# Kernel tuning notes

Measured on AMD Instinct MI355X. Metric: run time of the kernel, lower is better.

## Reference

```python
import jax, jax.numpy as jnp
import numpy as np

N, S, B, C = 8192, 13, 2, 3
EPS = 1e-6
LAMBDA_COORD, LAMBDA_OBJ, LAMBDA_NOOBJ, LAMBDA_CLASS = 5.0, 1.0, 0.5, 1.0


def setup_inputs() -> dict:
    key = jax.random.key(0)
    k1, k2, k3, k4 = jax.random.split(key, 4)
    predictions = jax.random.normal(k1, (N, S, S, B * (5 + C)), dtype=jnp.float32)
    xywh = jax.random.uniform(k2, (N, S, S, 4), dtype=jnp.float32)
    conf = (jax.random.uniform(k3, (N, S, S)) < 0.3).astype(jnp.float32)  # binary objectness
    cls_idx = jax.random.randint(k4, (N, S, S), 0, C)
    onehot = jax.nn.one_hot(cls_idx, C, dtype=jnp.float32)
    targets = jnp.concatenate(
        [xywh, conf[..., None], jnp.zeros((N, S, S, 5), jnp.float32), onehot], axis=-1
    )  # (N,S,S,13)
    return {"predictions": predictions, "targets": targets}


def reference(predictions, targets):
    batch = predictions.shape[0]
    mask = targets[..., 4] > 0  # (N,S,S) object-present mask
    m = mask.astype(predictions.dtype)

    # --- coord loss (box 0 only, as in the torch loop) ---
    px = jax.nn.sigmoid(predictions[..., 0])
    py = jax.nn.sigmoid(predictions[..., 1])
    pw, ph = predictions[..., 2], predictions[..., 3]
    tx, ty, tw, th = (targets[..., k] for k in range(4))
    coord = (
        (px - tx) ** 2
        + (py - ty) ** 2
        + (jnp.sqrt(jnp.abs(pw) + EPS) - jnp.sqrt(jnp.abs(tw) + EPS)) ** 2
        + (jnp.sqrt(jnp.abs(ph) + EPS) - jnp.sqrt(jnp.abs(th) + EPS)) ** 2
    )
    coord_loss = jnp.sum(m * coord)

    # --- objectness BCE (box 0) on object cells ---
    z = predictions[..., 4]
    tc = targets[..., 4]
    bce_obj = -(tc * jax.nn.log_sigmoid(z) + (1.0 - tc) * jax.nn.log_sigmoid(-z))
    conf_loss_obj = jnp.sum(m * bce_obj)

    # --- no-object BCE on both boxes (target 0) ---
    z_all = predictions[..., jnp.array([4, 9])]  # (N,S,S,B) conf logits
    bce_noobj = -jax.nn.log_sigmoid(-z_all)  # BCE(sigmoid(z), 0)
    conf_loss_noobj = jnp.sum((1.0 - m)[..., None] * bce_noobj)

    # --- class CE on object cells ---
    logits = predictions[..., B * 5 : B * 5 + C]  # (N,S,S,C)
    tcls = jnp.argmax(targets[..., B * 5 : B * 5 + C], axis=-1)
    ce = jax.nn.logsumexp(logits, axis=-1) - jnp.take_along_axis(
        logits, tcls[..., None], axis=-1
    )[..., 0]
    class_loss = jnp.sum(m * ce)

    # normalize by batch only if any such cell exists (matches torch branching)
    n_obj = jnp.sum(mask)
    n_noobj = mask.size - n_obj
    div_obj = jnp.where(n_obj > 0, 1.0 / batch, 1.0)
    div_noobj = jnp.where(n_noobj > 0, 1.0 / batch, 1.0)

    total = (
        LAMBDA_COORD * coord_loss * div_obj
        + LAMBDA_OBJ * conf_loss_obj * div_obj
        + LAMBDA_NOOBJ * conf_loss_noobj * div_noobj
        + LAMBDA_CLASS * class_loss * div_obj
    )
    return total
```

## Files before the change

### kernel.cpp

```cpp
#include <hip/hip_runtime.h>
#include <math.h>


#define EPSV 1e-6f

__global__ __launch_bounds__(256) void phobia_partial(
    const float* __restrict__ pred, const float* __restrict__ tgt,
    float* __restrict__ ws, long long cells)
{
    long long idx0 = (long long)blockIdx.x * blockDim.x + threadIdx.x;
    long long stride = (long long)gridDim.x * blockDim.x;

    float accA = 0.f;
    float accB = 0.f;
    float accC = 0.f;

    for (long long i = idx0; i < cells; i += stride) {
        const float* pr = pred + i * 16;
        const float* tr = tgt  + i * 13;

        float4 p03   = *reinterpret_cast<const float4*>(pr);
        float  p4    = pr[4];
        float  p9    = pr[9];
        float2 p1011 = *reinterpret_cast<const float2*>(pr + 10);
        float  p12   = pr[12];

        float t0 = tr[0], t1 = tr[1], t2 = tr[2], t3 = tr[3], t4 = tr[4];
        float t10 = tr[10], t11 = tr[11], t12 = tr[12];

        float m = (t4 > 0.f) ? 1.f : 0.f;

        float px = 1.f / (1.f + __expf(-p03.x));
        float py = 1.f / (1.f + __expf(-p03.y));
        float dx = px - t0;
        float dy = py - t1;
        float dw = sqrtf(fabsf(p03.z) + EPSV) - sqrtf(fabsf(t2) + EPSV);
        float dh = sqrtf(fabsf(p03.w) + EPSV) - sqrtf(fabsf(t3) + EPSV);
        float coord = dx*dx + dy*dy + dw*dw + dh*dh;

        float l1p4 = __logf(1.f + __expf(-fabsf(p4)));
        float logsig_p4 = fminf(p4, 0.f) - l1p4;
        float logsig_m4 = fminf(-p4, 0.f) - l1p4;
        float bce_obj = -(t4 * logsig_p4 + (1.f - t4) * logsig_m4);
        float bce_no4 = -logsig_m4;
        float bce_no9 = fmaxf(p9, 0.f) + __logf(1.f + __expf(-fabsf(p9)));

        int tcls = 0; float bt = t10;
        if (t11 > bt) { bt = t11; tcls = 1; }
        if (t12 > bt) { tcls = 2; }
        float lt = (tcls == 0) ? p1011.x : ((tcls == 1) ? p1011.y : p12);
        float mx = fmaxf(p1011.x, fmaxf(p1011.y, p12));
        float lse = mx + __logf(__expf(p1011.x - mx) + __expf(p1011.y - mx) + __expf(p12 - mx));
        float ce = lse - lt;

        accA += m * (5.f * coord + bce_obj + ce);
        accB += (1.f - m) * (bce_no4 + bce_no9);
        accC += m;
    }

    #pragma unroll
    for (int o = 32; o > 0; o >>= 1) {
        accA += __shfl_down(accA, o, 64);
        accB += __shfl_down(accB, o, 64);
        accC += __shfl_down(accC, o, 64);
    }
    __shared__ float sA[4], sB[4], sC[4];
    int wave = threadIdx.x >> 6;
    int lane = threadIdx.x & 63;
    if (lane == 0) { sA[wave] = accA; sB[wave] = accB; sC[wave] = accC; }
    __syncthreads();
    if (threadIdx.x == 0) {
        ws[blockIdx.x * 3 + 0] = sA[0] + sA[1] + sA[2] + sA[3];
        ws[blockIdx.x * 3 + 1] = sB[0] + sB[1] + sB[2] + sB[3];
        ws[blockIdx.x * 3 + 2] = sC[0] + sC[1] + sC[2] + sC[3];
    }
}

__global__ __launch_bounds__(1024) void phobia_final(
    const float* __restrict__ ws, int nblocks, float* __restrict__ out, long long cells)
{
    float a = 0.f, b = 0.f, c = 0.f;
    for (int i = threadIdx.x; i < nblocks; i += 1024) {
        a += ws[i * 3 + 0];
        b += ws[i * 3 + 1];
        c += ws[i * 3 + 2];
    }
    #pragma unroll
    for (int o = 32; o > 0; o >>= 1) {
        a += __shfl_down(a, o, 64);
        b += __shfl_down(b, o, 64);
        c += __shfl_down(c, o, 64);
    }
    __shared__ float sA[16], sB[16], sC[16];
    int wave = threadIdx.x >> 6;
    int lane = threadIdx.x & 63;
    if (lane == 0) { sA[wave] = a; sB[wave] = b; sC[wave] = c; }
    __syncthreads();
    if (threadIdx.x == 0) {
        float A = 0.f, B = 0.f, C = 0.f;
        #pragma unroll
        for (int w = 0; w < 16; ++w) { A += sA[w]; B += sB[w]; C += sC[w]; }
        float batch = (float)(cells / 169);
        float invb = 1.f / batch;
        float div_obj   = (C > 0.f) ? invb : 1.f;
        float div_noobj = (C < (float)cells) ? invb : 1.f;
        out[0] = A * div_obj + 0.5f * B * div_noobj;
    }
}

extern "C" void kernel_launch(void* const* d_in, const int* in_sizes, int n_in,
                              void* d_out, int out_size, void* d_ws, size_t ws_size,
                              hipStream_t stream) {
    const float* pred = (const float*)d_in[0];
    const float* tgt  = (const float*)d_in[1];
    float* out = (float*)d_out;
    float* ws  = (float*)d_ws;

    long long cells = (long long)in_sizes[0] / 16;

    int blocks = (int)((cells + 255) / 256);
    size_t need = (size_t)blocks * 3 * sizeof(float);
    while (need > ws_size && blocks > 1) { blocks >>= 1; need = (size_t)blocks * 3 * sizeof(float); }

    phobia_partial<<<blocks, 256, 0, stream>>>(pred, tgt, ws, cells);
    phobia_final<<<1, 1024, 0, stream>>>(ws, blocks, out, cells);
}
```

Baseline: 32.71 us.

## Stage prediction and target chunks through LDS with coalesced float4 loads

Each block now loads a 256-cell chunk of predictions and targets using fully coalesced float4 reads, scatters the needed prediction fields into shared memory, and then has each thread compute its cell from LDS. This replaces the strided per-thread loads, which fetched scattered fields with poor coalescing, especially for the 13-float target rows. In exchange it adds shared-memory traffic, two barriers per chunk, and LDS bank conflicts from the stride-9 and stride-13 layouts. It also assumes the cell count is a multiple of 256 and drops any tail.

```diff
diff --git a/kernel.cpp b/kernel.cpp
--- a/kernel.cpp
+++ b/kernel.cpp
@@ -3,39 +3,54 @@
 
 
 #define EPSV 1e-6f
+#define CHUNK 256
+#define NSLOT 9
 
 __global__ __launch_bounds__(256) void phobia_partial(
     const float* __restrict__ pred, const float* __restrict__ tgt,
-    float* __restrict__ ws, long long cells)
+    float* __restrict__ ws, int nchunks)
 {
-    long long idx0 = (long long)blockIdx.x * blockDim.x + threadIdx.x;
-    long long stride = (long long)gridDim.x * blockDim.x;
+    __shared__ float sp[CHUNK * NSLOT];
+    __shared__ float st[CHUNK * 13];
 
-    float accA = 0.f;
-    float accB = 0.f;
-    float accC = 0.f;
+    const int t = threadIdx.x;
+    float accA = 0.f, accB = 0.f, accC = 0.f;
 
-    for (long long i = idx0; i < cells; i += stride) {
-        const float* pr = pred + i * 16;
-        const float* tr = tgt  + i * 13;
+    for (int chunk = blockIdx.x; chunk < nchunks; chunk += gridDim.x) {
+        const float4* pf4 = reinterpret_cast<const float4*>(pred) + (size_t)chunk * (CHUNK * 4);
+        #pragma unroll
+        for (int s = 0; s < 4; ++s) {
+            int f = s * 256 + t;
+            float4 v = pf4[f];
+            int cell = f >> 2, quad = f & 3;
+            float* dst = &sp[cell * NSLOT];
+            if (quad == 0)      { dst[0] = v.x; dst[1] = v.y; dst[2] = v.z; dst[3] = v.w; }
+            else if (quad == 1) { dst[4] = v.x; }
+            else if (quad == 2) { dst[5] = v.y; dst[6] = v.z; dst[7] = v.w; }
+            else                { dst[8] = v.x; }
+        }
+        const float4* tf4 = reinterpret_cast<const float4*>(tgt) + (size_t)chunk * (CHUNK * 13 / 4);
+        float4* stf4 = reinterpret_cast<float4*>(st);
+        #pragma unroll
+        for (int s = 0; s < 3; ++s) stf4[s * 256 + t] = tf4[s * 256 + t];
+        if (t < 64) stf4[768 + t] = tf4[768 + t];
+        __syncthreads();
 
-        float4 p03   = *reinterpret_cast<const float4*>(pr);
-        float  p4    = pr[4];
-        float  p9    = pr[9];
-        float2 p1011 = *reinterpret_cast<const float2*>(pr + 10);
-        float  p12   = pr[12];
-
+        const float* pp = &sp[t * NSLOT];
+        const float* tr = &st[t * 13];
+        float p0 = pp[0], p1 = pp[1], p2 = pp[2], p3 = pp[3], p4 = pp[4];
+        float p9 = pp[5], p10 = pp[6], p11 = pp[7], p12 = pp[8];
         float t0 = tr[0], t1 = tr[1], t2 = tr[2], t3 = tr[3], t4 = tr[4];
         float t10 = tr[10], t11 = tr[11], t12 = tr[12];
 
         float m = (t4 > 0.f) ? 1.f : 0.f;
 
-        float px = 1.f / (1.f + __expf(-p03.x));
-        float py = 1.f / (1.f + __expf(-p03.y));
+        float px = 1.f / (1.f + __expf(-p0));
+        float py = 1.f / (1.f + __expf(-p1));
         float dx = px - t0;
         float dy = py - t1;
-        float dw = sqrtf(fabsf(p03.z) + EPSV) - sqrtf(fabsf(t2) + EPSV);
-        float dh = sqrtf(fabsf(p03.w) + EPSV) - sqrtf(fabsf(t3) + EPSV);
+        float dw = sqrtf(fabsf(p2) + EPSV) - sqrtf(fabsf(t2) + EPSV);
+        float dh = sqrtf(fabsf(p3) + EPSV) - sqrtf(fabsf(t3) + EPSV);
         float coord = dx*dx + dy*dy + dw*dw + dh*dh;
 
         float l1p4 = __logf(1.f + __expf(-fabsf(p4)));
@@ -48,14 +63,16 @@
         int tcls = 0; float bt = t10;
         if (t11 > bt) { bt = t11; tcls = 1; }
         if (t12 > bt) { tcls = 2; }
-        float lt = (tcls == 0) ? p1011.x : ((tcls == 1) ? p1011.y : p12);
-        float mx = fmaxf(p1011.x, fmaxf(p1011.y, p12));
-        float lse = mx + __logf(__expf(p1011.x - mx) + __expf(p1011.y - mx) + __expf(p12 - mx));
+        float lt = (tcls == 0) ? p10 : ((tcls == 1) ? p11 : p12);
+        float mx = fmaxf(p10, fmaxf(p11, p12));
+        float lse = mx + __logf(__expf(p10 - mx) + __expf(p11 - mx) + __expf(p12 - mx));
         float ce = lse - lt;
 
         accA += m * (5.f * coord + bce_obj + ce);
         accB += (1.f - m) * (bce_no4 + bce_no9);
         accC += m;
+
+        __syncthreads();
     }
 
     #pragma unroll
@@ -117,11 +134,12 @@
     float* ws  = (float*)d_ws;
 
     long long cells = (long long)in_sizes[0] / 16;
+    int nchunks = (int)(cells / CHUNK);
 
-    int blocks = (int)((cells + 255) / 256);
+    int blocks = nchunks;
     size_t need = (size_t)blocks * 3 * sizeof(float);
     while (need > ws_size && blocks > 1) { blocks >>= 1; need = (size_t)blocks * 3 * sizeof(float); }
 
-    phobia_partial<<<blocks, 256, 0, stream>>>(pred, tgt, ws, cells);
+    phobia_partial<<<blocks, 256, 0, stream>>>(pred, tgt, ws, nchunks);
     phobia_final<<<1, 1024, 0, stream>>>(ws, blocks, out, cells);
 }
```

After: 35.74 us. 1.09x slower.
